# Kernel optimization log

Hardware: AMD Instinct MI355X
Metric: run time of the kernel (lower is better)

Reference implementation:

```python
import jax, jax.numpy as jnp
import numpy as np

N_CLASS = 32000
EMB = 256
HID = 512
NUM_LAYER = 2
BATCH = 256
SEQ = 64


def setup_inputs() -> dict:
    key = jax.random.key(0)
    ks = jax.random.split(key, 16)
    s_e = 1.0 / np.sqrt(EMB)
    s_h = 1.0 / np.sqrt(HID)
    inp = {
        "X": jax.random.randint(ks[0], (BATCH, SEQ), 0, N_CLASS, dtype=jnp.int32),
        "C": jax.random.normal(ks[1], (N_CLASS, EMB), jnp.float32),
        # torch Linear weights are [out, in]; all layers share one set (list aliasing)
        "W_ii": jax.random.uniform(ks[2], (HID, EMB), jnp.float32, -s_e, s_e),
        "W_hi": jax.random.uniform(ks[3], (HID, HID), jnp.float32, -s_h, s_h),
        "b_i": jnp.ones((HID,), jnp.float32),
        "W_if": jax.random.uniform(ks[4], (HID, EMB), jnp.float32, -s_e, s_e),
        "W_hf": jax.random.uniform(ks[5], (HID, HID), jnp.float32, -s_h, s_h),
        "b_f": jnp.ones((HID,), jnp.float32),
        "W_ig": jax.random.uniform(ks[6], (HID, EMB), jnp.float32, -s_e, s_e),
        "W_hg": jax.random.uniform(ks[7], (HID, HID), jnp.float32, -s_h, s_h),
        "b_g": jnp.ones((HID,), jnp.float32),
        "W_io": jax.random.uniform(ks[8], (HID, EMB), jnp.float32, -s_e, s_e),
        "W_ho": jax.random.uniform(ks[9], (HID, HID), jnp.float32, -s_h, s_h),
        "b_o": jnp.ones((HID,), jnp.float32),
        "W": jax.random.uniform(ks[10], (EMB, HID), jnp.float32, -s_h, s_h),
        "b": jnp.ones((EMB,), jnp.float32),
        "W_final": jax.random.uniform(ks[11], (N_CLASS, HID), jnp.float32, -s_h, s_h),
        "b_final": jnp.ones((N_CLASS,), jnp.float32),
    }
    return inp


def _lstm_forward(X, C, W_ii, W_hi, b_i, W_if, W_hf, b_f, W_ig, W_hg, b_g,
                  W_io, W_ho, b_o, W, b, W_final, b_final):
    emb = C[X]                      # [B, S, E]
    xs = jnp.swapaxes(emb, 0, 1)    # [S, B, E] (time-major)
    B = X.shape[0]
    h0 = jnp.zeros((NUM_LAYER, B, HID), jnp.float32)
    c0 = jnp.zeros((NUM_LAYER, B, HID), jnp.float32)

    def step(carry, x_t):
        h, c = carry
        x = x_t
        hs, cs = [], []
        for l in range(NUM_LAYER):  # all layers share the same weights (aliased lists)
            i = jax.nn.sigmoid(x @ W_ii.T + h[l] @ W_hi.T + b_i)
            f = jax.nn.sigmoid(x @ W_if.T + h[l] @ W_hf.T + b_f)
            g = jnp.tanh(x @ W_ig.T + h[l] @ W_hg.T + b_g)
            o = jax.nn.sigmoid(x @ W_io.T + h[l] @ W_ho.T + b_o)
            c_new = f * c[l] + i * g
            h_new = o * jnp.tanh(c_new)
            x = h_new @ W.T + b      # project back to emb_size; dropout = identity (eval)
            hs.append(h_new)
            cs.append(c_new)
        return (jnp.stack(hs), jnp.stack(cs)), None

    (h, c), _ = jax.lax.scan(step, (h0, c0), xs)
    return h[-1] @ W_final.T + b_final   # [B, n_class]


def reference(X, C, W_ii, W_hi, b_i, W_if, W_hf, b_f, W_ig, W_hg, b_g,
              W_io, W_ho, b_o, W, b, W_final, b_final):
    return _lstm_forward(X, C, W_ii, W_hi, b_i, W_if, W_hf, b_f, W_ig, W_hg, b_g,
                         W_io, W_ho, b_o, W, b, W_final, b_final)
```

## Files before the change

### kernel.cpp

```cpp
#include <hip/hip_runtime.h>
#include <hip/hip_bf16.h>
#include <math.h>

#define B 256
#define S 64
#define E 256
#define H 512
#define NC 32000

typedef __attribute__((ext_vector_type(8))) short short8;
typedef __attribute__((ext_vector_type(4))) float f32x4;

__device__ inline short f2bf(float v) {
    __hip_bfloat16 h = __float2bfloat16(v);
    return *reinterpret_cast<short*>(&h);
}
__device__ inline float bf2f(short s) {
    __hip_bfloat16 h;
    *reinterpret_cast<short*>(&h) = s;
    return __bfloat162float(h);
}

__global__ __launch_bounds__(256) void k_zero(float4* __restrict__ p, int n4) {
    int i = blockIdx.x * 256 + threadIdx.x;
    if (i < n4) p[i] = float4{0.f, 0.f, 0.f, 0.f};
}

__global__ __launch_bounds__(256) void k_trans(const float* __restrict__ W0,
                                               const float* __restrict__ W1,
                                               const float* __restrict__ W2,
                                               const float* __restrict__ W3,
                                               int K, float* __restrict__ outT) {
    __shared__ float TT[64][65];
    const int u0 = blockIdx.x * 64;
    const int k0 = blockIdx.y * 64;
    const int g  = blockIdx.z;
    const float* Wg = (g == 0) ? W0 : (g == 1) ? W1 : (g == 2) ? W2 : W3;
    const int tx = threadIdx.x & 15, ty = threadIdx.x >> 4;
#pragma unroll
    for (int i = 0; i < 4; ++i) {
        float4 v = *(const float4*)(Wg + (size_t)(u0 + ty + i * 16) * K + k0 + tx * 4);
        TT[tx * 4 + 0][ty + i * 16] = v.x;
        TT[tx * 4 + 1][ty + i * 16] = v.y;
        TT[tx * 4 + 2][ty + i * 16] = v.z;
        TT[tx * 4 + 3][ty + i * 16] = v.w;
    }
    __syncthreads();
#pragma unroll
    for (int i = 0; i < 4; ++i) {
        int kl = ty + i * 16;
        float4 o = {TT[kl][tx * 4 + 0], TT[kl][tx * 4 + 1], TT[kl][tx * 4 + 2], TT[kl][tx * 4 + 3]};
        *(float4*)(outT + (size_t)(k0 + kl) * 2048 + g * 512 + u0 + tx * 4) = o;
    }
}

__global__ __launch_bounds__(256) void k_comb(const float* __restrict__ Wi0,
                                              const float* __restrict__ Wi1,
                                              const float* __restrict__ Wi2,
                                              const float* __restrict__ Wi3,
                                              const float* __restrict__ W,
                                              float* __restrict__ WcT) {
    __shared__ float WiS[64][65];
    __shared__ float WS[64][65];
    const int g  = blockIdx.x >> 3;
    const int u0 = (blockIdx.x & 7) * 64;
    const int k0 = blockIdx.y * 64;
    const float* Wi = (g == 0) ? Wi0 : (g == 1) ? Wi1 : (g == 2) ? Wi2 : Wi3;
    const int tx = threadIdx.x & 15, ty = threadIdx.x >> 4;
    float acc[4][4] = {};
    for (int e0 = 0; e0 < E; e0 += 64) {
#pragma unroll
        for (int i = 0; i < 4; ++i) {
            float4 v = *(const float4*)(Wi + (size_t)(u0 + ty + i * 16) * E + e0 + tx * 4);
            *(float4*)&WiS[ty + i * 16][tx * 4] = v;
        }
#pragma unroll
        for (int i = 0; i < 4; ++i) {
            float4 v = *(const float4*)(W + (size_t)(e0 + ty + i * 16) * H + k0 + tx * 4);
            *(float4*)&WS[ty + i * 16][tx * 4] = v;
        }
        __syncthreads();
#pragma unroll
        for (int el = 0; el < 64; ++el) {
            float uv[4], kv[4];
#pragma unroll
            for (int j = 0; j < 4; ++j) { uv[j] = WiS[ty * 4 + j][el]; kv[j] = WS[el][tx * 4 + j]; }
#pragma unroll
            for (int i2 = 0; i2 < 4; ++i2)
#pragma unroll
                for (int j = 0; j < 4; ++j) acc[i2][j] += uv[i2] * kv[j];
        }
        __syncthreads();
    }
#pragma unroll
    for (int j = 0; j < 4; ++j) {
        float4 o = {acc[0][j], acc[1][j], acc[2][j], acc[3][j]};
        *(float4*)(WcT + (size_t)(k0 + tx * 4 + j) * 2048 + g * 512 + u0 + ty * 4) = o;
    }
}

__global__ __launch_bounds__(256) void k_bias(const float* __restrict__ WxT,
                                              const float* __restrict__ bi,
                                              const float* __restrict__ bf_,
                                              const float* __restrict__ bg_,
                                              const float* __restrict__ bo_,
                                              const float* __restrict__ bvec,
                                              float* __restrict__ bias0,
                                              float* __restrict__ bias1) {
    int c = blockIdx.x * 256 + threadIdx.x;
    int g = c >> 9, u = c & 511;
    const float* bp = (g == 0) ? bi : (g == 1) ? bf_ : (g == 2) ? bg_ : bo_;
    float basev = bp[u];
    float s = 0.f;
    for (int e = 0; e < E; ++e) s += WxT[(size_t)e * 2048 + c] * bvec[e];
    bias0[c] = basev;
    bias1[c] = basev + s;
}

__global__ __launch_bounds__(256) void k_pack(const float* __restrict__ Wt,
                                              short* __restrict__ outp) {
    int idx = blockIdx.x * 256 + threadIdx.x;
    int k = idx >> 11, n = idx & 2047;
    float v = Wt[(size_t)k * 2048 + n];
    short hi = f2bf(v);
    short lo = f2bf(v - bf2f(hi));
    int kb = k >> 5, ks = (k >> 3) & 3, j = k & 7;
    int nb = n >> 4, nl = n & 15;
    int lane = ks * 16 + nl;
    size_t base = (((size_t)kb * 128 + nb) * 2) * 512 + (size_t)lane * 8 + j;
    outp[base] = hi;
    outp[base + 512] = lo;
}

__device__ __forceinline__ void gemm_h(const short* __restrict__ aH,
                                       const short* __restrict__ aL,
                                       const short* __restrict__ Bp,
                                       int ubG, int lane, int ks, f32x4 acc[4]) {
#pragma unroll 4
    for (int kb = 0; kb < 16; ++kb) {
        int ko = kb * 32 + ks * 8;
        short8 ahi = *(const short8*)(aH + ko);
        short8 alo = *(const short8*)(aL + ko);
#pragma unroll
        for (int g = 0; g < 4; ++g) {
            const short* bp = Bp + ((((size_t)kb * 4 + g) * 32) + ubG) * 1024 + (size_t)lane * 8;
            short8 bhi = *(const short8*)bp;
            short8 blo = *(const short8*)(bp + 512);
            acc[g] = __builtin_amdgcn_mfma_f32_16x16x32_bf16(ahi, bhi, acc[g], 0, 0, 0);
            acc[g] = __builtin_amdgcn_mfma_f32_16x16x32_bf16(alo, bhi, acc[g], 0, 0, 0);
            acc[g] = __builtin_amdgcn_mfma_f32_16x16x32_bf16(ahi, blo, acc[g], 0, 0, 0);
        }
    }
}

__global__ __launch_bounds__(256) void k_phase(int p, const int* __restrict__ X,
        const float* __restrict__ C,
        const short* __restrict__ WxP, const short* __restrict__ WcP,
        const short* __restrict__ WhP,
        const float* __restrict__ bias0g, const float* __restrict__ bias1g,
        short* __restrict__ h0H, short* __restrict__ h0L,
        short* __restrict__ h1H, short* __restrict__ h1L,
        float* __restrict__ c0, float* __restrict__ c1) {
    const int panel = blockIdx.y;
    if (panel == 0 && p >= S) return;
    if (panel == 1 && p == 0) return;
    const int tid  = threadIdx.x;
    const int wave = tid >> 6, lane = tid & 63;
    const int lrow = lane & 15, ks = lane >> 4;
    const int msup = blockIdx.x & 3;
    const int ubG  = blockIdx.x >> 2;
    const int row  = msup * 64 + wave * 16 + lrow;
    const int u    = ubG * 16 + lrow;

    f32x4 acc[4];
#pragma unroll
    for (int g = 0; g < 4; ++g) acc[g] = (f32x4){0.f, 0.f, 0.f, 0.f};

    if (panel == 0) {
        const int tok = X[row * S + p];
        const float* crow = C + (size_t)tok * E;
#pragma unroll 2
        for (int kb = 0; kb < 8; ++kb) {
            int ko = kb * 32 + ks * 8;
            float4 v0 = *(const float4*)(crow + ko);
            float4 v1 = *(const float4*)(crow + ko + 4);
            float v[8] = {v0.x, v0.y, v0.z, v0.w, v1.x, v1.y, v1.z, v1.w};
            short8 ahi, alo;
#pragma unroll
            for (int j = 0; j < 8; ++j) {
                short hj = f2bf(v[j]);
                ahi[j] = hj;
                alo[j] = f2bf(v[j] - bf2f(hj));
            }
#pragma unroll
            for (int g = 0; g < 4; ++g) {
                const short* bp = WxP + ((((size_t)kb * 4 + g) * 32) + ubG) * 1024 + (size_t)lane * 8;
                short8 bhi = *(const short8*)bp;
                short8 blo = *(const short8*)(bp + 512);
                acc[g] = __builtin_amdgcn_mfma_f32_16x16x32_bf16(ahi, bhi, acc[g], 0, 0, 0);
                acc[g] = __builtin_amdgcn_mfma_f32_16x16x32_bf16(alo, bhi, acc[g], 0, 0, 0);
                acc[g] = __builtin_amdgcn_mfma_f32_16x16x32_bf16(ahi, blo, acc[g], 0, 0, 0);
            }
        }
        size_t off = (size_t)((p + 1) & 1) * B * H + (size_t)row * H;
        gemm_h(h0H + off, h0L + off, WhP, ubG, lane, ks, acc);
    } else {
        const int q = p - 1;
        size_t offx = (size_t)(q & 1) * B * H + (size_t)row * H;
        gemm_h(h0H + offx, h0L + offx, WcP, ubG, lane, ks, acc);
        size_t offh = (size_t)((q + 1) & 1) * B * H + (size_t)row * H;
        gemm_h(h1H + offh, h1L + offh, WhP, ubG, lane, ks, acc);
    }

    short* dH; short* dL; float* cb;
    if (panel == 0) { size_t off = (size_t)(p & 1) * B * H; dH = h0H + off; dL = h0L + off; cb = c0; }
    else            { size_t off = (size_t)((p - 1) & 1) * B * H; dH = h1H + off; dL = h1L + off; cb = c1; }
    const float* bias = panel ? bias1g : bias0g;
    const float bI = bias[u], bF = bias[512 + u], bG = bias[1024 + u], bO = bias[1536 + u];
    const int rbase = msup * 64 + wave * 16 + ks * 4;
#pragma unroll
    for (int r = 0; r < 4; ++r) {
        size_t ix = (size_t)(rbase + r) * H + u;
        float pi = acc[0][r] + bI;
        float pf = acc[1][r] + bF;
        float pg = acc[2][r] + bG;
        float po = acc[3][r] + bO;
        float iv = 1.f / (1.f + expf(-pi));
        float fv = 1.f / (1.f + expf(-pf));
        float gv = tanhf(pg);
        float ov = 1.f / (1.f + expf(-po));
        float cn = fv * cb[ix] + iv * gv;
        float hn = ov * tanhf(cn);
        cb[ix] = cn;
        short hh = f2bf(hn);
        dH[ix] = hh;
        dL[ix] = f2bf(hn - bf2f(hh));
    }
}

__global__ __launch_bounds__(1024) void k_cls(const short* __restrict__ hH,
                                              const short* __restrict__ hL,
                                              const float* __restrict__ Wf,
                                              const float* __restrict__ bfin,
                                              float* __restrict__ out) {
    const int tid  = threadIdx.x;
    const int wave = tid >> 6, lane = tid & 63;
    const int lrow = lane & 15, ks = lane >> 4;
    const int n0 = blockIdx.x * 128;
    const int m0 = wave * 16;
    f32x4 acc[8];
#pragma unroll
    for (int nf = 0; nf < 8; ++nf) acc[nf] = (f32x4){0.f, 0.f, 0.f, 0.f};
    const short* aH = hH + (size_t)(m0 + lrow) * H;
    const short* aL = hL + (size_t)(m0 + lrow) * H;
#pragma unroll 2
    for (int kb = 0; kb < 16; ++kb) {
        int ko = kb * 32 + ks * 8;
        short8 ahi = *(const short8*)(aH + ko);
        short8 alo = *(const short8*)(aL + ko);
#pragma unroll
        for (int nf = 0; nf < 8; ++nf) {
            const float* wr = Wf + (size_t)(n0 + nf * 16 + lrow) * H + ko;
            float4 v0 = *(const float4*)wr;
            float4 v1 = *(const float4*)(wr + 4);
            short8 b;
            b[0] = f2bf(v0.x); b[1] = f2bf(v0.y); b[2] = f2bf(v0.z); b[3] = f2bf(v0.w);
            b[4] = f2bf(v1.x); b[5] = f2bf(v1.y); b[6] = f2bf(v1.z); b[7] = f2bf(v1.w);
            acc[nf] = __builtin_amdgcn_mfma_f32_16x16x32_bf16(ahi, b, acc[nf], 0, 0, 0);
            acc[nf] = __builtin_amdgcn_mfma_f32_16x16x32_bf16(alo, b, acc[nf], 0, 0, 0);
        }
    }
#pragma unroll
    for (int nf = 0; nf < 8; ++nf) {
        int n = n0 + nf * 16 + lrow;
        float bias = bfin[n];
#pragma unroll
        for (int r = 0; r < 4; ++r) {
            int brow = m0 + ks * 4 + r;
            out[(size_t)brow * NC + n] = acc[nf][r] + bias;
        }
    }
}

extern "C" void kernel_launch(void* const* d_in, const int* in_sizes, int n_in,
                              void* d_out, int out_size, void* d_ws, size_t ws_size,
                              hipStream_t stream) {
    const int*   X    = (const int*)d_in[0];
    const float* C    = (const float*)d_in[1];
    const float* Wii  = (const float*)d_in[2];
    const float* Whi  = (const float*)d_in[3];
    const float* bi   = (const float*)d_in[4];
    const float* Wif  = (const float*)d_in[5];
    const float* Whf  = (const float*)d_in[6];
    const float* bf   = (const float*)d_in[7];
    const float* Wig  = (const float*)d_in[8];
    const float* Whg  = (const float*)d_in[9];
    const float* bg   = (const float*)d_in[10];
    const float* Wio  = (const float*)d_in[11];
    const float* Who  = (const float*)d_in[12];
    const float* bo   = (const float*)d_in[13];
    const float* W    = (const float*)d_in[14];
    const float* bvec = (const float*)d_in[15];
    const float* Wf   = (const float*)d_in[16];
    const float* bfin = (const float*)d_in[17];
    float* out = (float*)d_out;
    char* base = (char*)d_ws;

    float* WhT  = (float*)(base + 0);
    float* WxT  = (float*)(base + 4194304);
    float* WcT  = (float*)(base + 6291456);
    short* WhP  = (short*)(base + 10485760);
    short* WxP  = (short*)(base + 14680064);
    short* WcP  = (short*)(base + 16777216);
    float* bias0 = (float*)(base + 20971520);
    float* bias1 = (float*)(base + 20979712);
    short* h0H  = (short*)(base + 20987904);
    short* h0L  = (short*)(base + 21512192);
    short* h1H  = (short*)(base + 22036480);
    short* h1L  = (short*)(base + 22560768);
    float* c0   = (float*)(base + 23085056);
    float* c1   = (float*)(base + 23609344);

    k_zero<<<768, 256, 0, stream>>>((float4*)(base + 20987904), 196608);

    k_trans<<<dim3(8, 8, 4), 256, 0, stream>>>(Whi, Whf, Whg, Who, H, WhT);
    k_trans<<<dim3(8, 4, 4), 256, 0, stream>>>(Wii, Wif, Wig, Wio, E, WxT);
    k_comb<<<dim3(32, 8), 256, 0, stream>>>(Wii, Wif, Wig, Wio, W, WcT);
    k_pack<<<4096, 256, 0, stream>>>(WhT, WhP);
    k_pack<<<2048, 256, 0, stream>>>(WxT, WxP);
    k_pack<<<4096, 256, 0, stream>>>(WcT, WcP);
    k_bias<<<8, 256, 0, stream>>>(WxT, bi, bf, bg, bo, bvec, bias0, bias1);

    for (int p = 0; p <= S; ++p)
        k_phase<<<dim3(128, 2), 256, 0, stream>>>(p, X, C, WxP, WcP, WhP, bias0, bias1,
                                                  h0H, h0L, h1H, h1L, c0, c1);

    k_cls<<<250, 1024, 0, stream>>>(h1H + (size_t)B * H, h1L + (size_t)B * H, Wf, bfin, out);
}
```

Measured before the change: 1.726 ms.

## Split K across waves in LSTM step kernel and stage classifier weights in LDS

The per-timestep kernel now launches 512 threads per block. Two groups of four waves each compute half of the K reduction, and their partial accumulators are combined through shared memory before the gate math runs. This doubles the waves in flight for the latency-bound recurrent step, at the cost of one barrier and an LDS round trip. Separately, the classifier kernel converts each 64-wide K chunk of W_final to bf16 once into swizzled LDS. All waves then read from LDS, instead of each wave re-reading and re-converting the same rows from global memory.

Result: faster. 1.621 ms (-6.1%).

```diff
diff --git a/kernel.cpp b/kernel.cpp
--- a/kernel.cpp
+++ b/kernel.cpp
@@ -132,12 +132,14 @@
     outp[base + 512] = lo;
 }
 
-__device__ __forceinline__ void gemm_h(const short* __restrict__ aH,
-                                       const short* __restrict__ aL,
-                                       const short* __restrict__ Bp,
-                                       int ubG, int lane, int ks, f32x4 acc[4]) {
+__device__ __forceinline__ void gemm_h_half(const short* __restrict__ aH,
+                                            const short* __restrict__ aL,
+                                            const short* __restrict__ Bp,
+                                            int ubG, int lane, int ks, int khalf,
+                                            f32x4 acc[4]) {
 #pragma unroll 4
-    for (int kb = 0; kb < 16; ++kb) {
+    for (int kb2 = 0; kb2 < 8; ++kb2) {
+        int kb = khalf * 8 + kb2;
         int ko = kb * 32 + ks * 8;
         short8 ahi = *(const short8*)(aH + ko);
         short8 alo = *(const short8*)(aL + ko);
@@ -153,7 +155,7 @@
     }
 }
 
-__global__ __launch_bounds__(256) void k_phase(int p, const int* __restrict__ X,
+__global__ __launch_bounds__(512) void k_phase(int p, const int* __restrict__ X,
         const float* __restrict__ C,
         const short* __restrict__ WxP, const short* __restrict__ WcP,
         const short* __restrict__ WhP,
@@ -164,13 +166,16 @@
     const int panel = blockIdx.y;
     if (panel == 0 && p >= S) return;
     if (panel == 1 && p == 0) return;
-    const int tid  = threadIdx.x;
-    const int wave = tid >> 6, lane = tid & 63;
-    const int lrow = lane & 15, ks = lane >> 4;
-    const int msup = blockIdx.x & 3;
-    const int ubG  = blockIdx.x >> 2;
-    const int row  = msup * 64 + wave * 16 + lrow;
-    const int u    = ubG * 16 + lrow;
+    const int tid   = threadIdx.x;
+    const int wave  = tid >> 6, lane = tid & 63;
+    const int khalf = wave >> 2, wsub = wave & 3;
+    const int lrow  = lane & 15, ks = lane >> 4;
+    const int msup  = blockIdx.x & 3;
+    const int ubG   = blockIdx.x >> 2;
+    const int row   = msup * 64 + wsub * 16 + lrow;
+    const int u     = ubG * 16 + lrow;
+
+    __shared__ float red[4][64][17];
 
     f32x4 acc[4];
 #pragma unroll
@@ -179,8 +184,9 @@
     if (panel == 0) {
         const int tok = X[row * S + p];
         const float* crow = C + (size_t)tok * E;
-#pragma unroll 2
-        for (int kb = 0; kb < 8; ++kb) {
+#pragma unroll
+        for (int kb2 = 0; kb2 < 4; ++kb2) {
+            int kb = khalf * 4 + kb2;
             int ko = kb * 32 + ks * 8;
             float4 v0 = *(const float4*)(crow + ko);
             float4 v1 = *(const float4*)(crow + ko + 4);
@@ -203,21 +209,35 @@
             }
         }
         size_t off = (size_t)((p + 1) & 1) * B * H + (size_t)row * H;
-        gemm_h(h0H + off, h0L + off, WhP, ubG, lane, ks, acc);
+        gemm_h_half(h0H + off, h0L + off, WhP, ubG, lane, ks, khalf, acc);
     } else {
         const int q = p - 1;
         size_t offx = (size_t)(q & 1) * B * H + (size_t)row * H;
-        gemm_h(h0H + offx, h0L + offx, WcP, ubG, lane, ks, acc);
+        gemm_h_half(h0H + offx, h0L + offx, WcP, ubG, lane, ks, khalf, acc);
         size_t offh = (size_t)((q + 1) & 1) * B * H + (size_t)row * H;
-        gemm_h(h1H + offh, h1L + offh, WhP, ubG, lane, ks, acc);
-    }
+        gemm_h_half(h1H + offh, h1L + offh, WhP, ubG, lane, ks, khalf, acc);
+    }
+
+    if (khalf == 1) {
+#pragma unroll
+        for (int g = 0; g < 4; ++g)
+#pragma unroll
+            for (int r = 0; r < 4; ++r) red[wsub][lane][g * 4 + r] = acc[g][r];
+    }
+    __syncthreads();
+    if (khalf == 1) return;
+
+#pragma unroll
+    for (int g = 0; g < 4; ++g)
+#pragma unroll
+        for (int r = 0; r < 4; ++r) acc[g][r] += red[wsub][lane][g * 4 + r];
 
     short* dH; short* dL; float* cb;
     if (panel == 0) { size_t off = (size_t)(p & 1) * B * H; dH = h0H + off; dL = h0L + off; cb = c0; }
     else            { size_t off = (size_t)((p - 1) & 1) * B * H; dH = h1H + off; dL = h1L + off; cb = c1; }
     const float* bias = panel ? bias1g : bias0g;
     const float bI = bias[u], bF = bias[512 + u], bG = bias[1024 + u], bO = bias[1536 + u];
-    const int rbase = msup * 64 + wave * 16 + ks * 4;
+    const int rbase = msup * 64 + wsub * 16 + ks * 4;
 #pragma unroll
     for (int r = 0; r < 4; ++r) {
         size_t ix = (size_t)(rbase + r) * H + u;
@@ -248,28 +268,47 @@
     const int lrow = lane & 15, ks = lane >> 4;
     const int n0 = blockIdx.x * 128;
     const int m0 = wave * 16;
+
+    __shared__ short BT[128 * 64];
+
     f32x4 acc[8];
 #pragma unroll
     for (int nf = 0; nf < 8; ++nf) acc[nf] = (f32x4){0.f, 0.f, 0.f, 0.f};
     const short* aH = hH + (size_t)(m0 + lrow) * H;
     const short* aL = hL + (size_t)(m0 + lrow) * H;
-#pragma unroll 2
-    for (int kb = 0; kb < 16; ++kb) {
-        int ko = kb * 32 + ks * 8;
-        short8 ahi = *(const short8*)(aH + ko);
-        short8 alo = *(const short8*)(aL + ko);
-#pragma unroll
-        for (int nf = 0; nf < 8; ++nf) {
-            const float* wr = Wf + (size_t)(n0 + nf * 16 + lrow) * H + ko;
+
+    const int rowl = tid >> 3;
+    const int kcol = (tid & 7) * 8;
+
+    for (int kc = 0; kc < 8; ++kc) {
+        {
+            const float* wr = Wf + (size_t)(n0 + rowl) * H + kc * 64 + kcol;
             float4 v0 = *(const float4*)wr;
             float4 v1 = *(const float4*)(wr + 4);
-            short8 b;
-            b[0] = f2bf(v0.x); b[1] = f2bf(v0.y); b[2] = f2bf(v0.z); b[3] = f2bf(v0.w);
-            b[4] = f2bf(v1.x); b[5] = f2bf(v1.y); b[6] = f2bf(v1.z); b[7] = f2bf(v1.w);
-            acc[nf] = __builtin_amdgcn_mfma_f32_16x16x32_bf16(ahi, b, acc[nf], 0, 0, 0);
-            acc[nf] = __builtin_amdgcn_mfma_f32_16x16x32_bf16(alo, b, acc[nf], 0, 0, 0);
-        }
-    }
+            short8 bw;
+            bw[0] = f2bf(v0.x); bw[1] = f2bf(v0.y); bw[2] = f2bf(v0.z); bw[3] = f2bf(v0.w);
+            bw[4] = f2bf(v1.x); bw[5] = f2bf(v1.y); bw[6] = f2bf(v1.z); bw[7] = f2bf(v1.w);
+            int byteoff = (rowl * 128 + kcol * 2) ^ ((rowl & 7) << 4);
+            *(short8*)((char*)BT + byteoff) = bw;
+        }
+        __syncthreads();
+#pragma unroll
+        for (int kbi = 0; kbi < 2; ++kbi) {
+            int ko = kc * 64 + kbi * 32 + ks * 8;
+            short8 ahi = *(const short8*)(aH + ko);
+            short8 alo = *(const short8*)(aL + ko);
+#pragma unroll
+            for (int nf = 0; nf < 8; ++nf) {
+                int nl = nf * 16 + lrow;
+                int byte = (nl * 128 + (kbi * 32 + ks * 8) * 2) ^ ((nl & 7) << 4);
+                short8 b = *(const short8*)((const char*)BT + byte);
+                acc[nf] = __builtin_amdgcn_mfma_f32_16x16x32_bf16(ahi, b, acc[nf], 0, 0, 0);
+                acc[nf] = __builtin_amdgcn_mfma_f32_16x16x32_bf16(alo, b, acc[nf], 0, 0, 0);
+            }
+        }
+        __syncthreads();
+    }
+
 #pragma unroll
     for (int nf = 0; nf < 8; ++nf) {
         int n = n0 + nf * 16 + lrow;
@@ -332,7 +371,7 @@
     k_bias<<<8, 256, 0, stream>>>(WxT, bi, bf, bg, bo, bvec, bias0, bias1);
 
     for (int p = 0; p <= S; ++p)
-        k_phase<<<dim3(128, 2), 256, 0, stream>>>(p, X, C, WxP, WcP, WhP, bias0, bias1,
+        k_phase<<<dim3(128, 2), 512, 0, stream>>>(p, X, C, WxP, WcP, WhP, bias0, bias1,
                                                   h0H, h0L, h1H, h1L, c0, c1);
 
     k_cls<<<250, 1024, 0, stream>>>(h1H + (size_t)B * H, h1L + (size_t)B * H, Wf, bfin, out);
```
